# Performance work log

Measured on AMD Instinct MI355X. Metric: run time of the kernel, lower is better.

## Reference

```python
import jax, jax.numpy as jnp
import numpy as np

PRECISION = 127.0  # number of discrete pulse-width levels per unit weight


def pwb_quantize(w):
    """PWBMapper: constrain weight to [-1, 1] and snap to `precision` levels."""
    return jnp.round(jnp.clip(w, -1.0, 1.0) * PRECISION) / PRECISION


def setup_inputs() -> dict:
    key = jax.random.key(0)
    kx, kw, kb = jax.random.split(key, 3)
    B, D_in, D_out = 32768, 1024, 128
    x = jax.random.normal(kx, (B, D_in), dtype=jnp.float32)
    # random_normal_initializer default stddev is small; scale a bit but keep in clip range
    W = jax.random.normal(kw, (D_in, D_out), dtype=jnp.float32) * 0.05
    b = jax.random.normal(kb, (D_out,), dtype=jnp.float32) * 0.05
    return {"x": x, "W": W, "b": b}


def reference(x, W, b):
    # Each neuron n.step(data) = dot(quantized weight column, data);
    # bias_neuron.step(e_i) = quantized bias[i].  Activation is identity (None).
    Wq = pwb_quantize(W)          # [D_in, D_out]
    bq = pwb_quantize(b)          # [D_out]
    return x @ Wq + bq            # [B, D_out]
```

## Files before the change

### kernel.cpp

```cpp
#include <hip/hip_runtime.h>
#include <cstdint>

#define K_DIM 1024
#define N_DIM 128
#define BM 64
#define BK 64

typedef __attribute__((ext_vector_type(8))) short bf16x8;
typedef __attribute__((ext_vector_type(4))) float f32x4;
typedef __attribute__((ext_vector_type(4))) int i32x4;
typedef unsigned short u16;
typedef unsigned int u32;

__device__ __forceinline__ float pwbq(float w) {
  w = fminf(fmaxf(w, -1.0f), 1.0f);
  return rintf(w * 127.0f) * (1.0f / 127.0f);
}

__device__ __forceinline__ u16 f2bf(float f) {
  union { float f; u32 u; } v; v.f = f;
  u32 r = v.u + 0x7FFFu + ((v.u >> 16) & 1u);
  return (u16)(r >> 16);
}

__global__ __launch_bounds__(256) void quantW_kernel(const float* __restrict__ W,
                                                     u16* __restrict__ Wt) {
  int e = blockIdx.x * 256 + threadIdx.x;
  int k = e >> 7;
  int n = e & 127;
  Wt[n * K_DIM + k] = f2bf(pwbq(W[e]));
}

template <bool PREQ>
__global__ __launch_bounds__(256, 2) void pwb_gemm(
    const float* __restrict__ x,
    const u16* __restrict__ Wt,
    const float* __restrict__ W,
    const float* __restrict__ bias,
    float* __restrict__ out) {

  __shared__ __align__(16) float As[2][BM * BK];
  __shared__ __align__(16) u16   Bs[2][N_DIM * 72];

  const int tid  = threadIdx.x;
  const int lane = tid & 63;
  const int wid  = tid >> 6;
  const int wm   = wid >> 1;
  const int wn   = wid & 1;
  const int m0   = blockIdx.x * BM;
  const int l15  = lane & 15;
  const int lg   = lane >> 4;

  auto stageA = [&](int s, int kt) {
    const float* xb = x + (size_t)m0 * K_DIM + kt * BK;
#pragma unroll
    for (int i = 0; i < 4; ++i) {
      int cd = i * 256 + tid;
      int cs = cd ^ ((cd >> 4) & 7);
      const float* src = xb + (cs >> 4) * K_DIM + (cs & 15) * 4;
      __builtin_amdgcn_global_load_lds(
          (const __attribute__((address_space(1))) void*)src,
          (__attribute__((address_space(3))) void*)(&As[s][cd * 4]),
          16, 0, 0);
    }
  };

  auto stageB = [&](int s, int kt) {
    const int n  = tid & 127;
    const int kh = tid >> 7;
    u16* dst = &Bs[s][n * 72 + kh * 32];
    if constexpr (PREQ) {
      const u16* src = Wt + (size_t)n * K_DIM + kt * BK + kh * 32;
      i32x4 v0 = *(const i32x4*)(src + 0);
      i32x4 v1 = *(const i32x4*)(src + 8);
      i32x4 v2 = *(const i32x4*)(src + 16);
      i32x4 v3 = *(const i32x4*)(src + 24);
      *(i32x4*)(dst + 0)  = v0;
      *(i32x4*)(dst + 8)  = v1;
      *(i32x4*)(dst + 16) = v2;
      *(i32x4*)(dst + 24) = v3;
    } else {
      const float* src = W + (size_t)(kt * BK + kh * 32) * N_DIM + n;
      union { i32x4 v[4]; u16 h[32]; } pk;
#pragma unroll
      for (int i = 0; i < 32; ++i) pk.h[i] = f2bf(pwbq(src[i * N_DIM]));
#pragma unroll
      for (int c = 0; c < 4; ++c) *(i32x4*)(dst + c * 8) = pk.v[c];
    }
  };

  f32x4 acc[2][4] = {};

  stageA(0, 0);
  stageB(0, 0);
  __syncthreads();

  const int NIT = K_DIM / BK;
#pragma unroll 2
  for (int kt = 0; kt < NIT; ++kt) {
    const int cur = kt & 1;
    if (kt + 1 < NIT) {
      stageA(cur ^ 1, kt + 1);
      stageB(cur ^ 1, kt + 1);
    }

#pragma unroll
    for (int kk = 0; kk < 2; ++kk) {
      bf16x8 a[2];
#pragma unroll
      for (int q = 0; q < 2; ++q) {
        int row  = wm * 32 + q * 16 + l15;
        int base = row * 256 + kk * 128 + lg * 32;
        int sw   = (row & 7) << 4;
        f32x4 f0 = *(const f32x4*)((const char*)&As[cur][0] + (base ^ sw));
        f32x4 f1 = *(const f32x4*)((const char*)&As[cur][0] + ((base + 16) ^ sw));
        union { bf16x8 v; u16 h[8]; } pa;
#pragma unroll
        for (int j = 0; j < 4; ++j) {
          pa.h[j]     = f2bf(f0[j]);
          pa.h[4 + j] = f2bf(f1[j]);
        }
        a[q] = pa.v;
      }
      bf16x8 bfr[4];
#pragma unroll
      for (int f = 0; f < 4; ++f) {
        int col = wn * 64 + f * 16 + l15;
        bfr[f] = *(const bf16x8*)(&Bs[cur][col * 72 + kk * 32 + lg * 8]);
      }
#pragma unroll
      for (int q = 0; q < 2; ++q)
#pragma unroll
        for (int f = 0; f < 4; ++f)
          acc[q][f] = __builtin_amdgcn_mfma_f32_16x16x32_bf16(a[q], bfr[f], acc[q][f], 0, 0, 0);
    }
    __syncthreads();
  }

  float bq[4];
#pragma unroll
  for (int f = 0; f < 4; ++f) bq[f] = pwbq(bias[wn * 64 + f * 16 + l15]);

#pragma unroll
  for (int q = 0; q < 2; ++q) {
    int gr0 = m0 + wm * 32 + q * 16 + lg * 4;
#pragma unroll
    for (int f = 0; f < 4; ++f) {
      int gc = wn * 64 + f * 16 + l15;
#pragma unroll
      for (int j = 0; j < 4; ++j) {
        out[(size_t)(gr0 + j) * N_DIM + gc] = acc[q][f][j] + bq[f];
      }
    }
  }
}

extern "C" void kernel_launch(void* const* d_in, const int* in_sizes, int n_in,
                              void* d_out, int out_size, void* d_ws, size_t ws_size,
                              hipStream_t stream) {
  const float* x = (const float*)d_in[0];
  const float* W = (const float*)d_in[1];
  const float* b = (const float*)d_in[2];
  float* out = (float*)d_out;

  const int M = in_sizes[0] / K_DIM;
  const int grid = M / BM;

  const size_t need = (size_t)K_DIM * N_DIM * sizeof(u16);
  if (d_ws != nullptr && ws_size >= need) {
    u16* Wt = (u16*)d_ws;
    quantW_kernel<<<(K_DIM * N_DIM) / 256, 256, 0, stream>>>(W, Wt);
    pwb_gemm<true><<<grid, 256, 0, stream>>>(x, Wt, nullptr, b, out);
  } else {
    pwb_gemm<false><<<grid, 256, 0, stream>>>(x, nullptr, W, b, out);
  }
}
```

Measured before the change: 40.10 us.

## Deepen GEMM pipeline to 4-stage ring with async LDS loads for both operands

The K tile shrinks to 32 and shared memory becomes a four-buffer ring with prefetch distance two, synchronised by explicit vmcnt waits and a single barrier per iteration instead of two __syncthreads. The weight quantisation kernel now writes a pre-swizzled per-tile image, so B tiles can also be copied straight into LDS with global_load_lds instead of going through registers. The fallback path is replaced by a simple naive kernel. This aims to hide more global-load latency and cut register staging, at the cost of more LDS and hand-tuned waitcnt counts that must match the number of issued loads exactly.

```diff
diff --git a/kernel.cpp b/kernel.cpp
--- a/kernel.cpp
+++ b/kernel.cpp
@@ -4,11 +4,11 @@
 #define K_DIM 1024
 #define N_DIM 128
 #define BM 64
-#define BK 64
+#define BK 32
+#define NT (K_DIM / BK)
 
 typedef __attribute__((ext_vector_type(8))) short bf16x8;
 typedef __attribute__((ext_vector_type(4))) float f32x4;
-typedef __attribute__((ext_vector_type(4))) int i32x4;
 typedef unsigned short u16;
 typedef unsigned int u32;
 
@@ -24,23 +24,37 @@
 }
 
 __global__ __launch_bounds__(256) void quantW_kernel(const float* __restrict__ W,
-                                                     u16* __restrict__ Wt) {
-  int e = blockIdx.x * 256 + threadIdx.x;
-  int k = e >> 7;
-  int n = e & 127;
-  Wt[n * K_DIM + k] = f2bf(pwbq(W[e]));
+                                                     u16* __restrict__ Wimg) {
+  int H = blockIdx.x * 256 + threadIdx.x;
+  int t = H >> 12;
+  int h = H & 4095;
+  int col = h >> 5;
+  int j = (h & 31) ^ ((col & 3) << 3);
+  int k = t * BK + j;
+  Wimg[H] = f2bf(pwbq(W[k * N_DIM + col]));
 }
 
-template <bool PREQ>
+__global__ __launch_bounds__(256) void naive_kernel(const float* __restrict__ x,
+                                                    const float* __restrict__ W,
+                                                    const float* __restrict__ b,
+                                                    float* __restrict__ out, int total) {
+  int idx = blockIdx.x * 256 + threadIdx.x;
+  if (idx >= total) return;
+  int m = idx >> 7, n = idx & 127;
+  float acc = pwbq(b[n]);
+  for (int k = 0; k < K_DIM; ++k)
+    acc = fmaf(x[(size_t)m * K_DIM + k], pwbq(W[k * N_DIM + n]), acc);
+  out[idx] = acc;
+}
+
 __global__ __launch_bounds__(256, 2) void pwb_gemm(
     const float* __restrict__ x,
-    const u16* __restrict__ Wt,
-    const float* __restrict__ W,
+    const u16* __restrict__ Wimg,
     const float* __restrict__ bias,
     float* __restrict__ out) {
 
-  __shared__ __align__(16) float As[2][BM * BK];
-  __shared__ __align__(16) u16   Bs[2][N_DIM * 72];
+  __shared__ __align__(16) float As[4][BM * BK];
+  __shared__ __align__(16) u16   Bs[4][N_DIM * BK];
 
   const int tid  = threadIdx.x;
   const int lane = tid & 63;
@@ -51,90 +65,75 @@
   const int l15  = lane & 15;
   const int lg   = lane >> 4;
 
-  auto stageA = [&](int s, int kt) {
-    const float* xb = x + (size_t)m0 * K_DIM + kt * BK;
+  auto stage = [&](int s, int t) {
 #pragma unroll
-    for (int i = 0; i < 4; ++i) {
+    for (int i = 0; i < 2; ++i) {
+      int cd  = i * 256 + tid;
+      int row = cd >> 3;
+      int cs  = (cd & 7) ^ (row & 7);
+      const float* srcA = x + (size_t)(m0 + row) * K_DIM + t * BK + cs * 4;
+      __builtin_amdgcn_global_load_lds(
+          (const __attribute__((address_space(1))) void*)srcA,
+          (__attribute__((address_space(3))) void*)(&As[s][cd * 4]), 16, 0, 0);
+    }
+#pragma unroll
+    for (int i = 0; i < 2; ++i) {
       int cd = i * 256 + tid;
-      int cs = cd ^ ((cd >> 4) & 7);
-      const float* src = xb + (cs >> 4) * K_DIM + (cs & 15) * 4;
+      const u16* srcB = Wimg + (size_t)t * (N_DIM * BK) + cd * 8;
       __builtin_amdgcn_global_load_lds(
-          (const __attribute__((address_space(1))) void*)src,
-          (__attribute__((address_space(3))) void*)(&As[s][cd * 4]),
-          16, 0, 0);
-    }
-  };
-
-  auto stageB = [&](int s, int kt) {
-    const int n  = tid & 127;
-    const int kh = tid >> 7;
-    u16* dst = &Bs[s][n * 72 + kh * 32];
-    if constexpr (PREQ) {
-      const u16* src = Wt + (size_t)n * K_DIM + kt * BK + kh * 32;
-      i32x4 v0 = *(const i32x4*)(src + 0);
-      i32x4 v1 = *(const i32x4*)(src + 8);
-      i32x4 v2 = *(const i32x4*)(src + 16);
-      i32x4 v3 = *(const i32x4*)(src + 24);
-      *(i32x4*)(dst + 0)  = v0;
-      *(i32x4*)(dst + 8)  = v1;
-      *(i32x4*)(dst + 16) = v2;
-      *(i32x4*)(dst + 24) = v3;
-    } else {
-      const float* src = W + (size_t)(kt * BK + kh * 32) * N_DIM + n;
-      union { i32x4 v[4]; u16 h[32]; } pk;
-#pragma unroll
-      for (int i = 0; i < 32; ++i) pk.h[i] = f2bf(pwbq(src[i * N_DIM]));
-#pragma unroll
-      for (int c = 0; c < 4; ++c) *(i32x4*)(dst + c * 8) = pk.v[c];
+          (const __attribute__((address_space(1))) void*)srcB,
+          (__attribute__((address_space(3))) void*)(&Bs[s][cd * 8]), 16, 0, 0);
     }
   };
 
   f32x4 acc[2][4] = {};
 
-  stageA(0, 0);
-  stageB(0, 0);
-  __syncthreads();
+  stage(0, 0);
+  stage(1, 1);
 
-  const int NIT = K_DIM / BK;
 #pragma unroll 2
-  for (int kt = 0; kt < NIT; ++kt) {
-    const int cur = kt & 1;
-    if (kt + 1 < NIT) {
-      stageA(cur ^ 1, kt + 1);
-      stageB(cur ^ 1, kt + 1);
+  for (int t = 0; t < NT; ++t) {
+    const int buf = t & 3;
+    if (t + 2 < NT) {
+      stage((t + 2) & 3, t + 2);
+      asm volatile("s_waitcnt vmcnt(8)" ::: "memory");
+    } else if (t + 1 < NT) {
+      asm volatile("s_waitcnt vmcnt(4)" ::: "memory");
+    } else {
+      asm volatile("s_waitcnt vmcnt(0)" ::: "memory");
+    }
+    asm volatile("s_barrier" ::: "memory");
+
+    bf16x8 a[2];
+#pragma unroll
+    for (int q = 0; q < 2; ++q) {
+      int row  = wm * 32 + q * 16 + l15;
+      int base = row * 128 + lg * 32;
+      int sw   = (row & 7) << 4;
+      f32x4 f0 = *(const f32x4*)((const char*)&As[buf][0] + (base ^ sw));
+      f32x4 f1 = *(const f32x4*)((const char*)&As[buf][0] + ((base + 16) ^ sw));
+      union { bf16x8 v; u16 h[8]; } pa;
+#pragma unroll
+      for (int j = 0; j < 4; ++j) {
+        pa.h[j]     = f2bf(f0[j]);
+        pa.h[4 + j] = f2bf(f1[j]);
+      }
+      a[q] = pa.v;
+    }
+
+    bf16x8 bfr[4];
+#pragma unroll
+    for (int f = 0; f < 4; ++f) {
+      int col  = wn * 64 + f * 16 + l15;
+      int hoff = col * 32 + ((lg * 8) ^ ((col & 3) << 3));
+      bfr[f] = *(const bf16x8*)(&Bs[buf][hoff]);
     }
 
 #pragma unroll
-    for (int kk = 0; kk < 2; ++kk) {
-      bf16x8 a[2];
+    for (int q = 0; q < 2; ++q)
 #pragma unroll
-      for (int q = 0; q < 2; ++q) {
-        int row  = wm * 32 + q * 16 + l15;
-        int base = row * 256 + kk * 128 + lg * 32;
-        int sw   = (row & 7) << 4;
-        f32x4 f0 = *(const f32x4*)((const char*)&As[cur][0] + (base ^ sw));
-        f32x4 f1 = *(const f32x4*)((const char*)&As[cur][0] + ((base + 16) ^ sw));
-        union { bf16x8 v; u16 h[8]; } pa;
-#pragma unroll
-        for (int j = 0; j < 4; ++j) {
-          pa.h[j]     = f2bf(f0[j]);
-          pa.h[4 + j] = f2bf(f1[j]);
-        }
-        a[q] = pa.v;
-      }
-      bf16x8 bfr[4];
-#pragma unroll
-      for (int f = 0; f < 4; ++f) {
-        int col = wn * 64 + f * 16 + l15;
-        bfr[f] = *(const bf16x8*)(&Bs[cur][col * 72 + kk * 32 + lg * 8]);
-      }
-#pragma unroll
-      for (int q = 0; q < 2; ++q)
-#pragma unroll
-        for (int f = 0; f < 4; ++f)
-          acc[q][f] = __builtin_amdgcn_mfma_f32_16x16x32_bf16(a[q], bfr[f], acc[q][f], 0, 0, 0);
-    }
-    __syncthreads();
+      for (int f = 0; f < 4; ++f)
+        acc[q][f] = __builtin_amdgcn_mfma_f32_16x16x32_bf16(a[q], bfr[f], acc[q][f], 0, 0, 0);
   }
 
   float bq[4];
@@ -168,10 +167,11 @@
 
   const size_t need = (size_t)K_DIM * N_DIM * sizeof(u16);
   if (d_ws != nullptr && ws_size >= need) {
-    u16* Wt = (u16*)d_ws;
-    quantW_kernel<<<(K_DIM * N_DIM) / 256, 256, 0, stream>>>(W, Wt);
-    pwb_gemm<true><<<grid, 256, 0, stream>>>(x, Wt, nullptr, b, out);
+    u16* Wimg = (u16*)d_ws;
+    quantW_kernel<<<(K_DIM * N_DIM) / 256, 256, 0, stream>>>(W, Wimg);
+    pwb_gemm<<<grid, 256, 0, stream>>>(x, Wimg, b, out);
   } else {
-    pwb_gemm<false><<<grid, 256, 0, stream>>>(x, nullptr, W, b, out);
+    int total = M * N_DIM;
+    naive_kernel<<<(total + 255) / 256, 256, 0, stream>>>(x, W, b, out, total);
   }
 }
```

Result: faster. 35.70 us (-11.0%).
